# Kernel optimization log

Hardware: AMD Instinct MI355X
Metric: run time of the kernel (lower is better)

The kernel has to match this reference:

```python
import jax, jax.numpy as jnp
import numpy as np

N = 50000
E = 300000
ATOM_DIM = 128
HID = 256
NODE_DIM = 64
NUM_LAYERS = 3
G = 2000  # number of graphs
LN_EPS = 1e-5


def setup_inputs() -> dict:
    key = jax.random.key(0)
    ks = jax.random.split(key, 12)
    x = jax.random.normal(ks[0], (N, ATOM_DIM), dtype=jnp.float32)
    edge_index = jax.random.randint(ks[1], (2, E), 0, N, dtype=jnp.int64)
    batch = jnp.sort(jax.random.randint(ks[2], (N,), 0, G, dtype=jnp.int64))
    s = 1.0 / np.sqrt(HID)
    W_enc = jax.random.normal(ks[3], (ATOM_DIM, HID), dtype=jnp.float32) * (1.0 / np.sqrt(ATOM_DIM))
    b_enc = jnp.zeros((HID,), dtype=jnp.float32)
    Ws = jax.random.normal(ks[4], (NUM_LAYERS, HID, HID), dtype=jnp.float32) * s
    bs = jnp.zeros((NUM_LAYERS, HID), dtype=jnp.float32)
    Wp = jax.random.normal(ks[5], (HID, NODE_DIM), dtype=jnp.float32) * s
    bp = jnp.zeros((NODE_DIM,), dtype=jnp.float32)
    gamma = jnp.ones((NODE_DIM,), dtype=jnp.float32)
    beta = jnp.zeros((NODE_DIM,), dtype=jnp.float32)
    return {"x": x, "edge_index": edge_index, "batch": batch,
            "W_enc": W_enc, "b_enc": b_enc, "Ws": Ws, "bs": bs,
            "Wp": Wp, "bp": bp, "gamma": gamma, "beta": beta}


def _gcn_conv(h, src, dst, dinv_src_dst, W, b):
    # h: [N, H]; PyG GCNConv: (D^-1/2 (A+I) D^-1/2) (h W) + b
    hw = h @ W                                      # [N, H]
    msg = hw[src] * dinv_src_dst[:, None]           # [E+N, H] gather + scale
    agg = jnp.zeros_like(hw).at[dst].add(msg)       # scatter-add to dst
    return agg + b


def reference(x, edge_index, batch, W_enc, b_enc, Ws, bs, Wp, bp, gamma, beta):
    n = x.shape[0]
    # add self loops (GCNConv default)
    loops = jnp.arange(n, dtype=edge_index.dtype)
    src = jnp.concatenate([edge_index[0], loops])
    dst = jnp.concatenate([edge_index[1], loops])
    # symmetric degree normalization computed on dst (PyG convention)
    deg = jax.ops.segment_sum(jnp.ones_like(dst, dtype=x.dtype), dst, num_segments=n)
    dinv = jnp.where(deg > 0, jax.lax.rsqrt(deg), 0.0)
    norm = dinv[src] * dinv[dst]                    # [E+N]

    h = x @ W_enc + b_enc                           # atom encoder
    for i in range(NUM_LAYERS):
        h = jax.nn.relu(_gcn_conv(h, src, dst, norm, Ws[i], bs[i]))
        # dropout is identity in eval mode

    # global_mean_pool over graph ids
    sums = jax.ops.segment_sum(h, batch, num_segments=G)          # [G, H]
    cnts = jax.ops.segment_sum(jnp.ones((n,), dtype=h.dtype), batch, num_segments=G)
    mol = sums / jnp.maximum(cnts, 1.0)[:, None]

    # projection: Linear -> LayerNorm
    p = mol @ Wp + bp                                # [G, NODE_DIM]
    mu = jnp.mean(p, axis=-1, keepdims=True)
    var = jnp.mean((p - mu) ** 2, axis=-1, keepdims=True)
    return (p - mu) * jax.lax.rsqrt(var + LN_EPS) * gamma + beta
```

## Files before the change

kernel.cpp:

```cpp
#include <hip/hip_runtime.h>
#include <hip/hip_bf16.h>

#define NN 50000
#define EE 300000
#define ATOM_DIM 128
#define HID 256
#define NODE_DIM 64
#define NUM_LAYERS 3
#define GG 2000
#define LN_EPS 1e-5f
#define CSRC_CAP 704512

typedef __attribute__((ext_vector_type(8))) short bf16x8;
typedef __attribute__((ext_vector_type(4))) float f32x4;

__device__ __forceinline__ ushort f2bf(float f) {
    __hip_bfloat16 h = __float2bfloat16(f);
    return *reinterpret_cast<ushort*>(&h);
}
__device__ __forceinline__ float bf2f(ushort u) {
    __hip_bfloat16 h = *reinterpret_cast<__hip_bfloat16*>(&u);
    return __bfloat162float(h);
}

__device__ __forceinline__ void gll16(const void* g, void* l) {
    __builtin_amdgcn_global_load_lds((const __attribute__((address_space(1))) unsigned int*)g,
                                     (__attribute__((address_space(3))) unsigned int*)l, 16, 0, 0);
}


#define PB_CVT   6250
#define PB_WTE   32
#define PB_WTL   192
#define PB_GB    8
#define PB_CSRC  688
#define PB_CNT   49
#define PB_ZROW  1
#define PB_TOTAL (PB_CVT + PB_WTE + PB_WTL + PB_GB + PB_CSRC + PB_CNT + PB_ZROW)

__device__ __forceinline__ void wt_tile(const float* __restrict__ W, ushort* __restrict__ Wt,
                                        int K, int N, int bx, int by) {
    __shared__ float t[32][33];
    int lx = threadIdx.x & 31, ly = threadIdx.x >> 5;
#pragma unroll
    for (int s = 0; s < 32; s += 8)
        t[ly + s][lx] = W[(size_t)(by * 32 + ly + s) * N + bx * 32 + lx];
    __syncthreads();
#pragma unroll
    for (int s = 0; s < 32; s += 8)
        Wt[(size_t)(bx * 32 + ly + s) * K + by * 32 + lx] = f2bf(t[lx][ly + s]);
}

__global__ __launch_bounds__(256) void k_prep(const float* __restrict__ x, ushort* __restrict__ xbf,
                                              const float* __restrict__ W_enc, ushort* __restrict__ wtE,
                                              const float* __restrict__ Ws, ushort* __restrict__ wtL,
                                              const int* __restrict__ batch, int* __restrict__ gstart,
                                              int* __restrict__ cnt, int* __restrict__ csrc,
                                              ushort* __restrict__ hbf_zero_row) {
    int b = blockIdx.x;
    int tid = threadIdx.x;
    if (b < PB_CVT) {
        int i = (b * 256 + tid) * 4;
        float4 v = *(const float4*)&x[i];
        ushort4 o;
        o.x = f2bf(v.x); o.y = f2bf(v.y); o.z = f2bf(v.z); o.w = f2bf(v.w);
        *(ushort4*)&xbf[i] = o;
        return;
    }
    b -= PB_CVT;
    if (b < PB_WTE) {
        wt_tile(W_enc, wtE, ATOM_DIM, HID, b & 7, b >> 3);
        return;
    }
    b -= PB_WTE;
    if (b < PB_WTL) {
        int z = b >> 6, r = b & 63;
        wt_tile(Ws + (size_t)z * HID * HID, wtL + (size_t)z * HID * HID, HID, HID, r & 7, r >> 3);
        return;
    }
    b -= PB_WTL;
    if (b < PB_GB) {
        int g = b * 256 + tid;
        if (g > GG) return;
        int lo = 0, hi = NN;
        while (lo < hi) { int mid = (lo + hi) >> 1; if (batch[mid] < g) lo = mid + 1; else hi = mid; }
        gstart[g] = lo;
        return;
    }
    b -= PB_GB;
    if (b < PB_CSRC) {
        int i = (b * 256 + tid) * 4;
        if (i < CSRC_CAP) *(int4*)&csrc[i] = make_int4(NN, NN, NN, NN);
        return;
    }
    b -= PB_CSRC;
    if (b < PB_CNT) {
        int i = (b * 256 + tid) * 4;
        if (i < NN) *(int4*)&cnt[i] = make_int4(0, 0, 0, 0);
        return;
    }
    hbf_zero_row[tid] = 0;
}


__global__ __launch_bounds__(256) void k_count(const int* __restrict__ ei, int* cnt, int e_total) {
    int e = blockIdx.x * 256 + threadIdx.x;
    if (e < e_total) atomicAdd(&cnt[ei[e_total + e]], 1);
}

__global__ __launch_bounds__(256) void k_scan1(const int* __restrict__ cnt, int* __restrict__ rowp,
                                               int* __restrict__ csum, int n) {
    __shared__ int s[256];
    int tid = threadIdx.x;
    int base = blockIdx.x * 1024 + tid * 4;
    int v[4];
#pragma unroll
    for (int j = 0; j < 4; ++j) { int i = base + j; v[j] = (i < n) ? ((cnt[i] + 8) & ~7) : 0; }
    int tsum = v[0] + v[1] + v[2] + v[3];
    s[tid] = tsum;
    __syncthreads();
    for (int off = 1; off < 256; off <<= 1) {
        int t = (tid >= off) ? s[tid - off] : 0;
        __syncthreads();
        s[tid] += t;
        __syncthreads();
    }
    int excl = s[tid] - tsum;
#pragma unroll
    for (int j = 0; j < 4; ++j) { int i = base + j; if (i < n) rowp[i] = excl; excl += v[j]; }
    if (tid == 255) csum[blockIdx.x] = s[255];
}

__global__ __launch_bounds__(256) void k_scan2(int* __restrict__ rowp, int* __restrict__ fill,
                                               const int* __restrict__ csum, const int* __restrict__ cnt,
                                               float* __restrict__ dinv, int n) {
    __shared__ int soff;
    int chunk = blockIdx.x;
    if (threadIdx.x == 0) {
        int o = 0;
        for (int c = 0; c < chunk; ++c) o += csum[c];
        soff = o;
    }
    __syncthreads();
    int off = soff;
    int base = chunk * 1024 + threadIdx.x * 4;
#pragma unroll
    for (int j = 0; j < 4; ++j) {
        int i = base + j;
        if (i < n) {
            int r = rowp[i] + off;
            rowp[i] = r; fill[i] = r;
            dinv[i] = rsqrtf((float)(cnt[i] + 1));
        }
    }
    if (chunk == gridDim.x - 1 && threadIdx.x == 255) rowp[n] = off + csum[chunk];
}

__global__ __launch_bounds__(256) void k_fill(const int* __restrict__ ei, int* fill, int* __restrict__ csrc,
                                              int e_total, int n) {
    int e = blockIdx.x * 256 + threadIdx.x;
    int tot = e_total + n;
    if (e >= tot) return;
    int s, d;
    if (e < e_total) { s = ei[e]; d = ei[e_total + e]; }
    else { s = d = e - e_total; }
    int pos = atomicAdd(&fill[d], 1);
    csrc[pos] = s;
}


__global__ __launch_bounds__(256) void k_gemm_bf16(const ushort* __restrict__ A, const ushort* __restrict__ Bt,
                                                   const float* __restrict__ bias, ushort* __restrict__ Cb,
                                                   const float* __restrict__ dscale, int relu,
                                                   int M, int K, int NC) {
    __shared__ short As[2][4096];
    __shared__ short Bs[2][4096];
    int tid = threadIdx.x;
    int lane = tid & 63, w = tid >> 6;
    int wr = w >> 1, wc = w & 1;
    int row0 = blockIdx.y * 128, col0 = blockIdx.x * 128;

    f32x4 acc[4][4] = {};

    int r15 = lane & 15;
    int swz = ((r15 >> 1) & 3) << 3;
    int koff = ((lane >> 4) << 3) ^ swz;

    const ushort* aB[2];
    const ushort* bB[2];
#pragma unroll
    for (int i = 0; i < 2; ++i) {
        int row = i * 64 + (tid >> 2);
        int cg = (tid & 3) ^ ((row >> 1) & 3);
        int ra = row0 + row; if (ra > M - 1) ra = M - 1;
        aB[i] = A + (size_t)ra * K + cg * 8;
        bB[i] = Bt + (size_t)(col0 + row) * K + cg * 8;
    }
    int ldst = w * 512;

#define STAGE(buf, kk) do { int k0_ = (kk) << 5;                      \
        gll16(aB[0] + k0_, &As[buf][ldst]);                           \
        gll16(aB[1] + k0_, &As[buf][2048 + ldst]);                    \
        gll16(bB[0] + k0_, &Bs[buf][ldst]);                           \
        gll16(bB[1] + k0_, &Bs[buf][2048 + ldst]);                    \
    } while (0)

#define COMPUTE(buf) do {                                                              \
        bf16x8 af[4], bfr[4];                                                          \
        _Pragma("unroll")                                                              \
        for (int m = 0; m < 4; ++m)                                                    \
            af[m] = *(const bf16x8*)&As[buf][(wr * 64 + m * 16 + r15) * 32 + koff];    \
        _Pragma("unroll")                                                              \
        for (int n = 0; n < 4; ++n)                                                    \
            bfr[n] = *(const bf16x8*)&Bs[buf][(wc * 64 + n * 16 + r15) * 32 + koff];   \
        _Pragma("unroll")                                                              \
        for (int m = 0; m < 4; ++m)                                                    \
            _Pragma("unroll")                                                          \
            for (int n = 0; n < 4; ++n)                                                \
                acc[m][n] = __builtin_amdgcn_mfma_f32_16x16x32_bf16(af[m], bfr[n], acc[m][n], 0, 0, 0); \
    } while (0)

    int nk = K >> 5;
    STAGE(0, 0);
    __syncthreads();
    for (int t = 0; t < nk - 1; ++t) {
        int buf = t & 1;
        STAGE(buf ^ 1, t + 1);
        COMPUTE(buf);
        __syncthreads();
    }
    COMPUTE((nk - 1) & 1);

#undef STAGE
#undef COMPUTE

    int cc = lane & 15, rq = (lane >> 4) * 4;
#pragma unroll
    for (int m = 0; m < 4; ++m) {
#pragma unroll
        for (int r = 0; r < 4; ++r) {
            int gr = row0 + wr * 64 + m * 16 + rq + r;
            if (gr >= M) continue;
            float ds = dscale ? dscale[gr] : 1.0f;
#pragma unroll
            for (int n = 0; n < 4; ++n) {
                int gc = col0 + wc * 64 + n * 16 + cc;
                float v = acc[m][n][r];
                if (bias) v += bias[gc];
                if (relu) v = fmaxf(v, 0.f);
                Cb[(size_t)gr * NC + gc] = f2bf(v * ds);
            }
        }
    }
}


__global__ __launch_bounds__(256) void k_aggregate_bf(const ushort* __restrict__ hin,
                                                      const int* __restrict__ rowp,
                                                      const int* __restrict__ csrc,
                                                      const float* __restrict__ dinv,
                                                      ushort* __restrict__ aout, int n) {
    int wave = threadIdx.x >> 6, lane = threadIdx.x & 63;
    int node = blockIdx.x * 4 + wave;
    if (node >= n) return;
    int beg = __builtin_amdgcn_readfirstlane(rowp[node]);
    int end = __builtin_amdgcn_readfirstlane(rowp[node + 1]);
    const ushort* hc = hin + lane * 4;
    float4 acc = make_float4(0.f, 0.f, 0.f, 0.f);
    for (int j = beg; j < end; j += 8) {
        int s0 = csrc[j + 0], s1 = csrc[j + 1], s2 = csrc[j + 2], s3 = csrc[j + 3];
        int s4 = csrc[j + 4], s5 = csrc[j + 5], s6 = csrc[j + 6], s7 = csrc[j + 7];
        ushort4 r0 = *(const ushort4*)&hc[(size_t)s0 * HID];
        ushort4 r1 = *(const ushort4*)&hc[(size_t)s1 * HID];
        ushort4 r2 = *(const ushort4*)&hc[(size_t)s2 * HID];
        ushort4 r3 = *(const ushort4*)&hc[(size_t)s3 * HID];
        ushort4 r4 = *(const ushort4*)&hc[(size_t)s4 * HID];
        ushort4 r5 = *(const ushort4*)&hc[(size_t)s5 * HID];
        ushort4 r6 = *(const ushort4*)&hc[(size_t)s6 * HID];
        ushort4 r7 = *(const ushort4*)&hc[(size_t)s7 * HID];
        acc.x += ((bf2f(r0.x) + bf2f(r1.x)) + (bf2f(r2.x) + bf2f(r3.x))) +
                 ((bf2f(r4.x) + bf2f(r5.x)) + (bf2f(r6.x) + bf2f(r7.x)));
        acc.y += ((bf2f(r0.y) + bf2f(r1.y)) + (bf2f(r2.y) + bf2f(r3.y))) +
                 ((bf2f(r4.y) + bf2f(r5.y)) + (bf2f(r6.y) + bf2f(r7.y)));
        acc.z += ((bf2f(r0.z) + bf2f(r1.z)) + (bf2f(r2.z) + bf2f(r3.z))) +
                 ((bf2f(r4.z) + bf2f(r5.z)) + (bf2f(r6.z) + bf2f(r7.z)));
        acc.w += ((bf2f(r0.w) + bf2f(r1.w)) + (bf2f(r2.w) + bf2f(r3.w))) +
                 ((bf2f(r4.w) + bf2f(r5.w)) + (bf2f(r6.w) + bf2f(r7.w)));
    }
    float dn = dinv[node];
    ushort4 o;
    o.x = f2bf(dn * acc.x); o.y = f2bf(dn * acc.y);
    o.z = f2bf(dn * acc.z); o.w = f2bf(dn * acc.w);
    *(ushort4*)&aout[(size_t)node * HID + lane * 4] = o;
}


__global__ __launch_bounds__(256) void k_pool_proj_ln(const ushort* __restrict__ hbf, const int* __restrict__ gstart,
                                                      const float* __restrict__ Wp, const float* __restrict__ bp,
                                                      const float* __restrict__ gamma, const float* __restrict__ beta,
                                                      float* __restrict__ out) {
    __shared__ float mol[HID];
    __shared__ float part[4][NODE_DIM];
    int g = blockIdx.x;
    int t = threadIdx.x;
    int beg = gstart[g], end = gstart[g + 1];
    float sum = 0.f;
    for (int r = beg; r < end; ++r) sum += bf2f(hbf[(size_t)r * HID + t]);
    float inv = 1.0f / fmaxf((float)(end - beg), 1.0f);
    mol[t] = sum * inv;
    __syncthreads();
    int w = t >> 6, j = t & 63;
    float p = 0.f;
    int k0 = w * 64;
#pragma unroll 8
    for (int k = 0; k < 64; ++k) p += mol[k0 + k] * Wp[(size_t)(k0 + k) * NODE_DIM + j];
    part[w][j] = p;
    __syncthreads();
    if (t < 64) {
        float pj = part[0][j] + part[1][j] + part[2][j] + part[3][j] + bp[j];
        float s = pj;
#pragma unroll
        for (int m = 1; m < 64; m <<= 1) s += __shfl_xor(s, m);
        float mu = s * (1.0f / 64.0f);
        float d = pj - mu;
        float vs = d * d;
#pragma unroll
        for (int m = 1; m < 64; m <<= 1) vs += __shfl_xor(vs, m);
        out[(size_t)g * NODE_DIM + j] = d * rsqrtf(vs * (1.0f / 64.0f) + LN_EPS) * gamma[j] + beta[j];
    }
}


extern "C" void kernel_launch(void* const* d_in, const int* in_sizes, int n_in,
                              void* d_out, int out_size, void* d_ws, size_t ws_size,
                              hipStream_t stream) {
    const float* x     = (const float*)d_in[0];
    const int*   ei    = (const int*)d_in[1];
    const int*   batch = (const int*)d_in[2];
    const float* W_enc = (const float*)d_in[3];
    const float* b_enc = (const float*)d_in[4];
    const float* Ws    = (const float*)d_in[5];
    const float* bs    = (const float*)d_in[6];
    const float* Wp    = (const float*)d_in[7];
    const float* bp    = (const float*)d_in[8];
    const float* gamma = (const float*)d_in[9];
    const float* beta  = (const float*)d_in[10];
    float* out = (float*)d_out;

    ushort* hbf  = (ushort*)d_ws;
    ushort* abf  = hbf + (size_t)(NN + 1) * HID;
    ushort* xbf  = abf + (size_t)NN * HID;
    ushort* wtE  = xbf + (size_t)NN * ATOM_DIM;
    ushort* wtL  = wtE + HID * ATOM_DIM;
    float*  dinv = (float*)(wtL + (size_t)NUM_LAYERS * HID * HID);
    int* cnt    = (int*)(dinv + NN);
    int* rowp   = cnt + NN;
    int* fill   = rowp + NN + 1;
    int* csrc   = fill + NN;
    int* csum   = csrc + CSRC_CAP;
    int* gstart = csum + 64;

    const int EN = EE + NN;
    const int NCH = (NN + 1023) / 1024;

    k_prep<<<PB_TOTAL, 256, 0, stream>>>(x, xbf, W_enc, wtE, Ws, wtL, batch, gstart,
                                         cnt, csrc, hbf + (size_t)NN * HID);

    k_count<<<(EE + 255) / 256, 256, 0, stream>>>(ei, cnt, EE);
    k_scan1<<<NCH, 256, 0, stream>>>(cnt, rowp, csum, NN);
    k_scan2<<<NCH, 256, 0, stream>>>(rowp, fill, csum, cnt, dinv, NN);
    k_fill<<<(EN + 255) / 256, 256, 0, stream>>>(ei, fill, csrc, EE, NN);

    dim3 ggrid(HID / 128, (NN + 127) / 128);

    k_gemm_bf16<<<ggrid, 256, 0, stream>>>(xbf, wtE, b_enc, hbf, dinv, 0, NN, ATOM_DIM, HID);

    for (int l = 0; l < NUM_LAYERS; ++l) {
        k_aggregate_bf<<<(NN + 3) / 4, 256, 0, stream>>>(hbf, rowp, csrc, dinv, abf, NN);
        const float* ds = (l < NUM_LAYERS - 1) ? dinv : nullptr;
        k_gemm_bf16<<<ggrid, 256, 0, stream>>>(abf, wtL + (size_t)l * HID * HID, bs + (size_t)l * HID,
                                               hbf, ds, 1, NN, HID, HID);
    }

    k_pool_proj_ln<<<GG, 256, 0, stream>>>(hbf, gstart, Wp, bp, gamma, beta, out);
}
```

Measured before the change: 298.6 us.

## Triple-buffer GEMM LDS with vmcnt waits and compile-time K unrolling

Turns the bf16 MFMA GEMM from a double-buffered loop into a three-stage LDS pipeline. Loads run two k-tiles ahead, and each iteration waits only for the oldest group with explicit s_waitcnt vmcnt and a single barrier. K becomes a template parameter so the k-loop fully unrolls. The aim is to hide global-to-LDS latency and drop one barrier per iteration, at the cost of 50% more shared memory per block, which may lower occupancy.

```diff
diff --git a/kernel.cpp b/kernel.cpp
--- a/kernel.cpp
+++ b/kernel.cpp
@@ -169,12 +169,16 @@
 }
 
 
-__global__ __launch_bounds__(256) void k_gemm_bf16(const ushort* __restrict__ A, const ushort* __restrict__ Bt,
-                                                   const float* __restrict__ bias, ushort* __restrict__ Cb,
+template <int K>
+__global__ __launch_bounds__(256) void k_gemm_pipe(const ushort* __restrict__ A,
+                                                   const ushort* __restrict__ Bt,
+                                                   const float* __restrict__ bias,
+                                                   ushort* __restrict__ Cb,
                                                    const float* __restrict__ dscale, int relu,
-                                                   int M, int K, int NC) {
-    __shared__ short As[2][4096];
-    __shared__ short Bs[2][4096];
+                                                   int M) {
+    constexpr int NK = K / 32;
+    __shared__ short As[3][4096];
+    __shared__ short Bs[3][4096];
     int tid = threadIdx.x;
     int lane = tid & 63, w = tid >> 6;
     int wr = w >> 1, wc = w & 1;
@@ -220,16 +224,16 @@
                 acc[m][n] = __builtin_amdgcn_mfma_f32_16x16x32_bf16(af[m], bfr[n], acc[m][n], 0, 0, 0); \
     } while (0)
 
-    int nk = K >> 5;
     STAGE(0, 0);
-    __syncthreads();
-    for (int t = 0; t < nk - 1; ++t) {
-        int buf = t & 1;
-        STAGE(buf ^ 1, t + 1);
-        COMPUTE(buf);
-        __syncthreads();
-    }
-    COMPUTE((nk - 1) & 1);
+    STAGE(1, 1);
+#pragma unroll
+    for (int t = 0; t < NK; ++t) {
+        if (t < NK - 1) asm volatile("s_waitcnt vmcnt(4)" ::: "memory");
+        else            asm volatile("s_waitcnt vmcnt(0)" ::: "memory");
+        __builtin_amdgcn_s_barrier();
+        if (t + 2 < NK) STAGE((t + 2) % 3, t + 2);
+        COMPUTE(t % 3);
+    }
 
 #undef STAGE
 #undef COMPUTE
@@ -248,7 +252,7 @@
                 float v = acc[m][n][r];
                 if (bias) v += bias[gc];
                 if (relu) v = fmaxf(v, 0.f);
-                Cb[(size_t)gr * NC + gc] = f2bf(v * ds);
+                Cb[(size_t)gr * HID + gc] = f2bf(v * ds);
             }
         }
     }
@@ -373,13 +377,13 @@
 
     dim3 ggrid(HID / 128, (NN + 127) / 128);
 
-    k_gemm_bf16<<<ggrid, 256, 0, stream>>>(xbf, wtE, b_enc, hbf, dinv, 0, NN, ATOM_DIM, HID);
+    k_gemm_pipe<ATOM_DIM><<<ggrid, 256, 0, stream>>>(xbf, wtE, b_enc, hbf, dinv, 0, NN);
 
     for (int l = 0; l < NUM_LAYERS; ++l) {
         k_aggregate_bf<<<(NN + 3) / 4, 256, 0, stream>>>(hbf, rowp, csrc, dinv, abf, NN);
         const float* ds = (l < NUM_LAYERS - 1) ? dinv : nullptr;
-        k_gemm_bf16<<<ggrid, 256, 0, stream>>>(abf, wtL + (size_t)l * HID * HID, bs + (size_t)l * HID,
-                                               hbf, ds, 1, NN, HID, HID);
+        k_gemm_pipe<HID><<<ggrid, 256, 0, stream>>>(abf, wtL + (size_t)l * HID * HID,
+                                                    bs + (size_t)l * HID, hbf, ds, 1, NN);
     }
 
     k_pool_proj_ln<<<GG, 256, 0, stream>>>(hbf, gstart, Wp, bp, gamma, beta, out);
```

Result: no change. 293.9 us (-1.6%).
